# Optimization experiments

Hardware: AMD Instinct MI355X
Metric: run time of the kernel (lower is better)

Reference implementation:

```python
import jax, jax.numpy as jnp
import numpy as np

B, S, D, H = 2, 2048, 1024, 16
HD = D // H  # head_dim = 64
ROPE_BASE = 10000.0


def _rope_cos_sin(seq_len, head_dim, dtype=jnp.float32):
    inv_freq = 1.0 / (ROPE_BASE ** (jnp.arange(0, head_dim, 2, dtype=jnp.float32) / head_dim))
    t = jnp.arange(seq_len, dtype=jnp.float32)
    freqs = jnp.einsum('i,j->ij', t, inv_freq)          # [S, HD/2]
    emb = jnp.concatenate([freqs, freqs], axis=-1)       # [S, HD]
    return jnp.cos(emb).astype(dtype), jnp.sin(emb).astype(dtype)


def _rotate_half(x):
    x1, x2 = jnp.split(x, 2, axis=-1)
    return jnp.concatenate([-x2, x1], axis=-1)


def setup_inputs() -> dict:
    key = jax.random.key(0)
    ks = jax.random.split(key, 5)
    scale = 1.0 / np.sqrt(D)
    return {
        'hidden_states': jax.random.normal(ks[0], (B, S, D), dtype=jnp.float32),
        'Wq': jax.random.normal(ks[1], (D, D), dtype=jnp.float32) * scale,
        'Wk': jax.random.normal(ks[2], (D, D), dtype=jnp.float32) * scale,
        'Wv': jax.random.normal(ks[3], (D, D), dtype=jnp.float32) * scale,
        'Wo': jax.random.normal(ks[4], (D, D), dtype=jnp.float32) * scale,
    }


def reference(hidden_states, Wq, Wk, Wv, Wo):
    b, s, d = hidden_states.shape
    # torch nn.Linear(weight W) computes x @ W^T
    q = hidden_states @ Wq.T
    k = hidden_states @ Wk.T
    v = hidden_states @ Wv.T
    # [B, H, S, HD]
    q = q.reshape(b, s, H, HD).transpose(0, 2, 1, 3)
    k = k.reshape(b, s, H, HD).transpose(0, 2, 1, 3)
    v = v.reshape(b, s, H, HD).transpose(0, 2, 1, 3)
    cos, sin = _rope_cos_sin(s, HD, q.dtype)  # [S, HD]
    cos = cos[None, None]  # [1,1,S,HD]
    sin = sin[None, None]
    q = q * cos + _rotate_half(q) * sin
    k = k * cos + _rotate_half(k) * sin
    scale = HD ** -0.5
    attn = jnp.einsum('bhqd,bhkd->bhqk', q, k) * scale
    attn = jax.nn.softmax(attn.astype(jnp.float32), axis=-1).astype(q.dtype)
    out = jnp.einsum('bhqk,bhkd->bhqd', attn, v)
    out = out.transpose(0, 2, 1, 3).reshape(b, s, d)
    return out @ Wo.T
```

## Files before the change

### kernel.cpp

```cpp
#include <hip/hip_runtime.h>
#include <math.h>

constexpr int Bc = 2;
constexpr int Sc = 2048;
constexpr int Dc = 1024;
constexpr int Hc = 16;
constexpr int HDc = 64;

constexpr float QSC = 0.125f * 1.4426950408889634f;

typedef __attribute__((ext_vector_type(8))) short bf16x8;
typedef __attribute__((ext_vector_type(4))) float f32x4;
typedef __attribute__((ext_vector_type(4))) unsigned short us4;
typedef __attribute__((ext_vector_type(2))) unsigned int u32x2;
typedef __attribute__((ext_vector_type(4))) unsigned int u32x4;

typedef const __attribute__((address_space(1))) unsigned int* gp_t;
typedef __attribute__((address_space(3))) unsigned int* lp_t;

__device__ __forceinline__ unsigned f2bf(float x) {
    unsigned u = __float_as_uint(x);
    return (u + 0x7FFFu + ((u >> 16) & 1u)) >> 16;
}

__device__ __forceinline__ void split2(float x, unsigned short& h, unsigned short& l) {
    unsigned hh = f2bf(x);
    h = (unsigned short)hh;
    l = (unsigned short)f2bf(x - __uint_as_float(hh << 16));
}

#if __has_builtin(__builtin_amdgcn_permlane32_swap)
__device__ __forceinline__ void plswap32(unsigned& a, unsigned& b) {
    u32x2 r = __builtin_amdgcn_permlane32_swap(a, b, false, false);
    a = r.x; b = r.y;
}
#else
__device__ __forceinline__ void plswap32(unsigned& a, unsigned& b) {
    asm volatile("v_permlane32_swap_b32 %0, %1" : "+v"(a), "+v"(b));
}
#endif
#if __has_builtin(__builtin_amdgcn_permlane16_swap)
__device__ __forceinline__ void plswap16(unsigned& a, unsigned& b) {
    u32x2 r = __builtin_amdgcn_permlane16_swap(a, b, false, false);
    a = r.x; b = r.y;
}
#else
__device__ __forceinline__ void plswap16(unsigned& a, unsigned& b) {
    asm volatile("v_permlane16_swap_b32 %0, %1" : "+v"(a), "+v"(b));
}
#endif

__device__ __forceinline__ void exppack(const f32x4& sv, unsigned& w0, unsigned& w1) {
    unsigned u0 = __float_as_uint(__builtin_amdgcn_exp2f(sv[0]));
    unsigned u1 = __float_as_uint(__builtin_amdgcn_exp2f(sv[1]));
    unsigned u2 = __float_as_uint(__builtin_amdgcn_exp2f(sv[2]));
    unsigned u3 = __float_as_uint(__builtin_amdgcn_exp2f(sv[3]));
    w0 = __builtin_amdgcn_perm(u1, u0, 0x07060302u);
    w1 = __builtin_amdgcn_perm(u3, u2, 0x07060302u);
}

__global__ void rope_table(float* __restrict__ ct, float* __restrict__ st_) {
    int id = blockIdx.x * 256 + threadIdx.x;
    int s = id >> 5;
    int i = id & 31;
    double invf = pow(10000.0, -(double)i / 32.0);
    double ang = (double)s * invf;
    ct[id] = (float)cos(ang);
    st_[id] = (float)sin(ang);
}

__global__ void split_xw(const float* __restrict__ x,
                         const float* __restrict__ Wq, const float* __restrict__ Wk,
                         const float* __restrict__ Wv, const float* __restrict__ Wo,
                         unsigned short* __restrict__ xh,
                         unsigned short* __restrict__ whAll, unsigned short* __restrict__ wlAll) {
    int y = blockIdx.y;
    const float* src;
    unsigned short* h;
    unsigned short* l = nullptr;
    int n;
    if (y == 0) { src = x; h = xh; n = 1 << 22; }
    else {
        src = (y == 1) ? Wq : (y == 2) ? Wk : (y == 3) ? Wv : Wo;
        h = whAll + (size_t)(y - 1) * (1 << 20);
        if (y == 4) l = wlAll + (size_t)3 * (1 << 20);
        n = 1 << 20;
    }
    int i = (blockIdx.x * 256 + threadIdx.x) * 4;
    if (i >= n) return;
    float4 v = *(const float4*)(src + i);
    us4 hh;
    ((unsigned short*)&hh)[0] = (unsigned short)f2bf(v.x);
    ((unsigned short*)&hh)[1] = (unsigned short)f2bf(v.y);
    ((unsigned short*)&hh)[2] = (unsigned short)f2bf(v.z);
    ((unsigned short*)&hh)[3] = (unsigned short)f2bf(v.w);
    *(us4*)(h + i) = hh;
    if (l) {
        us4 ll;
        const float* vp = (const float*)&v;
#pragma unroll
        for (int e = 0; e < 4; e++) {
            unsigned short hi = ((unsigned short*)&hh)[e];
            ((unsigned short*)&ll)[e] =
                (unsigned short)f2bf(vp[e] - __uint_as_float((unsigned)hi << 16));
        }
        *(us4*)(l + i) = ll;
    }
}

__global__ __launch_bounds__(512, 4) void gemm_qkv9(
    const unsigned short* __restrict__ Ah,
    const unsigned short* __restrict__ whAll,
    unsigned short* __restrict__ Qh,
    unsigned short* __restrict__ Kh,
    unsigned short* __restrict__ Vh,
    const float* __restrict__ ct, const float* __restrict__ st_) {
    constexpr int K = 1024;
    __shared__ __align__(16) unsigned short As[2][8192], Bs[2][8192];

    const int t = threadIdx.x;
    const int lane = t & 63;
    const int wave = t >> 6;
    const int l15 = lane & 15;
    const int quad = lane >> 4;
    const int wr = wave >> 1;
    const int wc = wave & 1;
    const int m0 = blockIdx.x * 128;
    const int n0 = blockIdx.y * 128;
    const int z = blockIdx.z;
    const unsigned short* Wh = whAll + (size_t)z * (1 << 20);

    const int c0 = t,        r0 = c0 >> 3, s0 = c0 & 7;
    const int c1 = t + 512,  r1 = c1 >> 3, s1 = c1 & 7;
    const unsigned short* gA0 = Ah + (size_t)(m0 + r0) * K + (s0 ^ (r0 & 7)) * 8;
    const unsigned short* gA1 = Ah + (size_t)(m0 + r1) * K + (s1 ^ (r1 & 7)) * 8;
    const unsigned short* gB0 = Wh + (size_t)(n0 + r0) * K + (s0 ^ (r0 & 7)) * 8;
    const unsigned short* gB1 = Wh + (size_t)(n0 + r1) * K + (s1 ^ (r1 & 7)) * 8;
    const int d0 = c0 * 8, d1 = c1 * 8;

    f32x4 acc[2][4];
#pragma unroll
    for (int i = 0; i < 2; i++)
#pragma unroll
        for (int j = 0; j < 4; j++) acc[i][j] = (f32x4){0.f, 0.f, 0.f, 0.f};

#define STGQ(X) do {                                                                       \
        const int _ko = (X) * 64;                                                          \
        const int _bf = (X) & 1;                                                           \
        __builtin_amdgcn_global_load_lds((gp_t)(gA0 + _ko), (lp_t)(&As[_bf][d0]), 16, 0, 0); \
        __builtin_amdgcn_global_load_lds((gp_t)(gA1 + _ko), (lp_t)(&As[_bf][d1]), 16, 0, 0); \
        __builtin_amdgcn_global_load_lds((gp_t)(gB0 + _ko), (lp_t)(&Bs[_bf][d0]), 16, 0, 0); \
        __builtin_amdgcn_global_load_lds((gp_t)(gB1 + _ko), (lp_t)(&Bs[_bf][d1]), 16, 0, 0); \
    } while (0)

    STGQ(0);

    for (int it = 0; it < 16; ++it) {
        __syncthreads();
        if (it + 1 < 16) STGQ(it + 1);
        const unsigned short* a = &As[it & 1][0];
        const unsigned short* bb = &Bs[it & 1][0];
#pragma unroll
        for (int ks = 0; ks < 2; ks++) {
            bf16x8 ah[2], bh[4];
#pragma unroll
            for (int i = 0; i < 2; i++) {
                int row = wr * 32 + i * 16 + l15;
                ah[i] = *(const bf16x8*)&a[row * 64 + ((ks * 4 + quad) ^ (row & 7)) * 8];
            }
#pragma unroll
            for (int j = 0; j < 4; j++) {
                int row = wc * 64 + j * 16 + l15;
                bh[j] = *(const bf16x8*)&bb[row * 64 + ((ks * 4 + quad) ^ (row & 7)) * 8];
            }
#pragma unroll
            for (int i = 0; i < 2; i++)
#pragma unroll
                for (int j = 0; j < 4; j++)
                    acc[i][j] = __builtin_amdgcn_mfma_f32_16x16x32_bf16(ah[i], bh[j], acc[i][j], 0, 0, 0);
        }
    }
#undef STGQ

    const int hcol = blockIdx.y * 2 + wc;
    if (z == 2) {
#pragma unroll
        for (int i = 0; i < 2; i++) {
            int m_base = m0 + wr * 32 + i * 16 + quad * 4;
            int bbk = m_base >> 11;
            int T = (m_base & (Sc - 1)) >> 6;
            int ii = (2 * wr + i) & 3;
            int kk = ii >> 1;
            int qd = ((ii & 1) << 1) | (quad >> 1);
            int tj = (quad & 1) * 4;
            size_t tilebase = (((size_t)(bbk * Hc + hcol)) * 32 + T) * 4096;
#pragma unroll
            for (int jj = 0; jj < 4; jj++) {
                int d = jj * 16 + l15;
                size_t off = tilebase + (size_t)(((kk * 4 + qd) * 64 + d) * 8 + tj);
                us4 v4;
#pragma unroll
                for (int r = 0; r < 4; r++)
                    ((unsigned short*)&v4)[r] = (unsigned short)f2bf(acc[i][jj][r]);
                *(us4*)(Vh + off) = v4;
            }
        }
    } else {
#pragma unroll
        for (int i = 0; i < 2; i++)
#pragma unroll
            for (int r = 0; r < 4; r++) {
                int m = m0 + wr * 32 + i * 16 + quad * 4 + r;
                int bbk = m >> 11, s = m & (Sc - 1);
#pragma unroll
                for (int jp = 0; jp < 2; jp++) {
                    int d = jp * 16 + l15;
                    float cs = ct[s * 32 + d];
                    float sn = st_[s * 32 + d];
                    float x0 = acc[i][jp][r];
                    float x1 = acc[i][jp + 2][r];
                    float y0 = x0 * cs - x1 * sn;
                    float y1 = x1 * cs + x0 * sn;
                    if (z == 0) {
                        size_t rowb = (((size_t)(bbk * Hc + hcol)) * Sc + s) * HDc;
                        Qh[rowb + d]      = (unsigned short)f2bf(y0 * QSC);
                        Qh[rowb + d + 32] = (unsigned short)f2bf(y1 * QSC);
                    } else {
                        int T = s >> 6, tok = s & 63;
                        size_t tb = (((size_t)(bbk * Hc + hcol)) * 32 + T) * 8;
                        size_t off0 = ((tb + (d >> 3)) * 64 + tok) * 8 + (d & 7);
                        size_t off1 = ((tb + (d >> 3) + 4) * 64 + tok) * 8 + (d & 7);
                        Kh[off0] = (unsigned short)f2bf(y0);
                        Kh[off1] = (unsigned short)f2bf(y1);
                    }
                }
            }
    }
}

__global__ __launch_bounds__(512) void attn11(
    const unsigned short* __restrict__ Qh,
    const unsigned short* __restrict__ Kh,
    const unsigned short* __restrict__ Vh,
    unsigned short* __restrict__ AOh, unsigned short* __restrict__ AOl) {
    __shared__ __align__(16) unsigned short KsH[3 * 4096], VtH[3 * 4096];

    const int t = threadIdx.x;
    const int lane = t & 63;
    const int wave = t >> 6;
    const int l = lane & 15;
    const int quad = lane >> 4;
    const int id = blockIdx.x;
    const int bh = (id & 7) * 4 + (id >> 7);
    const int qt = (id >> 3) & 15;
    const int q0 = qt * 128;
    const int b = bh >> 4;
    const int hh = bh & 15;

    const bf16x8 ONES8 = {(short)0x3F80, (short)0x3F80, (short)0x3F80, (short)0x3F80,
                          (short)0x3F80, (short)0x3F80, (short)0x3F80, (short)0x3F80};

    bf16x8 qf[2];
    {
        size_t rowb = ((size_t)bh * Sc + q0 + wave * 16 + l) * HDc;
#pragma unroll
        for (int ks = 0; ks < 2; ks++)
            qf[ks] = *(const bf16x8*)(Qh + rowb + ks * 32 + quad * 8);
    }

    f32x4 o[4], lac;
    lac = (f32x4){0.f, 0.f, 0.f, 0.f};
#pragma unroll
    for (int i = 0; i < 4; i++) o[i] = (f32x4){0.f, 0.f, 0.f, 0.f};

    const int tensor = wave >> 2;
    const int coff0 = (wave * 2) & 7;
    unsigned short* larr = tensor ? VtH : KsH;
    const unsigned short* gT =
        (tensor ? Vh : Kh) + (size_t)bh * Sc * HDc + coff0 * 512 + lane * 8;

#pragma unroll
    for (int q = 0; q < 2; q++)
        __builtin_amdgcn_global_load_lds(
            (gp_t)(gT + q * 512),
            (lp_t)(larr + coff0 * 512 + q * 512),
            16, 0, 0);

    int bc = 0;
    for (int kt = 0; kt < 32; kt++) {
        if (kt + 1 < 32) {
            int nb = bc + 1; if (nb == 3) nb = 0;
            const unsigned short* g = gT + (size_t)(kt + 1) * 4096;
            unsigned short* dst = larr + nb * 4096 + coff0 * 512;
#pragma unroll
            for (int q = 0; q < 2; q++)
                __builtin_amdgcn_global_load_lds(
                    (gp_t)(g + q * 512),
                    (lp_t)(dst + q * 512),
                    16, 0, 0);
            asm volatile("s_waitcnt vmcnt(2)" ::: "memory");
        } else {
            asm volatile("s_waitcnt vmcnt(0)" ::: "memory");
        }
        __builtin_amdgcn_s_barrier();
        const unsigned short* Kbuf = KsH + bc * 4096;
        const unsigned short* Vbuf = VtH + bc * 4096;

        f32x4 s[4];
#pragma unroll
        for (int tt = 0; tt < 4; tt++) s[tt] = (f32x4){0.f, 0.f, 0.f, 0.f};
        __builtin_amdgcn_s_setprio(1);
#pragma unroll
        for (int ks = 0; ks < 2; ks++)
#pragma unroll
            for (int tt = 0; tt < 4; tt++) {
                bf16x8 kf = *(const bf16x8*)&Kbuf[((ks * 4 + quad) * 64 + tt * 16 + l) * 8];
                s[tt] = __builtin_amdgcn_mfma_f32_16x16x32_bf16(kf, qf[ks], s[tt], 0, 0, 0);
            }
        __builtin_amdgcn_s_setprio(0);

        bf16x8 pf[2];
#pragma unroll
        for (int ttp = 0; ttp < 2; ttp++) {
            unsigned A0, A1, B0, B1;
            exppack(s[2 * ttp], A0, A1);
            exppack(s[2 * ttp + 1], B0, B1);
            plswap32(A0, B0);
            plswap16(A0, B0);
            plswap32(A1, B1);
            plswap16(A1, B1);
            u32x4 fw = {A0, A1, B0, B1};
            bf16x8 p8 = __builtin_bit_cast(bf16x8, fw);
            pf[ttp] = p8;
            lac = __builtin_amdgcn_mfma_f32_16x16x32_bf16(ONES8, p8, lac, 0, 0, 0);
        }

        __builtin_amdgcn_s_setprio(1);
#pragma unroll
        for (int kk = 0; kk < 2; kk++)
#pragma unroll
            for (int dd = 0; dd < 4; dd++) {
                bf16x8 vf = *(const bf16x8*)
                    &Vbuf[(size_t)((kk * 4 + quad) * 64 + dd * 16 + l) * 8];
                o[dd] = __builtin_amdgcn_mfma_f32_16x16x32_bf16(vf, pf[kk], o[dd], 0, 0, 0);
            }
        __builtin_amdgcn_s_setprio(0);
        if (++bc == 3) bc = 0;
    }

    {
        float inv = 1.f / lac[0];
        int q = q0 + wave * 16 + l;
        size_t rowb = ((size_t)b * Sc + q) * Dc + hh * HDc + quad * 4;
#pragma unroll
        for (int dd = 0; dd < 4; dd++) {
            us4 h4, l4;
#pragma unroll
            for (int r = 0; r < 4; r++)
                split2(o[dd][r] * inv,
                       ((unsigned short*)&h4)[r], ((unsigned short*)&l4)[r]);
            *(us4*)(AOh + rowb + dd * 16) = h4;
            *(us4*)(AOl + rowb + dd * 16) = l4;
        }
    }
}

__global__ __launch_bounds__(512, 4) void gemm_out9(
    const unsigned short* __restrict__ Ah, const unsigned short* __restrict__ Al,
    const unsigned short* __restrict__ Wh, const unsigned short* __restrict__ Wl,
    float* __restrict__ C0, float* __restrict__ C1) {
    constexpr int K = 1024;
    __shared__ __align__(16) unsigned short AsH[2][4096], AsL[2][4096],
                                            BsH[2][4096], BsL[2][4096];

    const int t = threadIdx.x;
    const int lane = t & 63;
    const int wave = t >> 6;
    const int l15 = lane & 15;
    const int quad = lane >> 4;
    const int wr = wave >> 1;
    const int wc = wave & 1;
    const int m0 = blockIdx.x * 128;
    const int n0 = blockIdx.y * 128;
    const int k0 = blockIdx.z * 512;
    float* __restrict__ C = blockIdx.z ? C1 : C0;

    const int rr = t >> 2, ss = t & 3;
    const int gc = (ss ^ (rr & 3)) * 8;
    const unsigned short* gah = Ah + (size_t)(m0 + rr) * K + k0 + gc;
    const unsigned short* gal = Al + (size_t)(m0 + rr) * K + k0 + gc;
    const unsigned short* gbh = Wh + (size_t)(n0 + rr) * K + k0 + gc;
    const unsigned short* gbl = Wl + (size_t)(n0 + rr) * K + k0 + gc;
    const int dd_ = t * 8;

    f32x4 acc[2][4];
#pragma unroll
    for (int i = 0; i < 2; i++)
#pragma unroll
        for (int j = 0; j < 4; j++) acc[i][j] = (f32x4){0.f, 0.f, 0.f, 0.f};

#define STGO(X) do {                                                                       \
        const int _ko = (X) * 32;                                                          \
        const int _bf = (X) & 1;                                                           \
        __builtin_amdgcn_global_load_lds((gp_t)(gah + _ko), (lp_t)(&AsH[_bf][dd_]), 16, 0, 0); \
        __builtin_amdgcn_global_load_lds((gp_t)(gal + _ko), (lp_t)(&AsL[_bf][dd_]), 16, 0, 0); \
        __builtin_amdgcn_global_load_lds((gp_t)(gbh + _ko), (lp_t)(&BsH[_bf][dd_]), 16, 0, 0); \
        __builtin_amdgcn_global_load_lds((gp_t)(gbl + _ko), (lp_t)(&BsL[_bf][dd_]), 16, 0, 0); \
    } while (0)

    STGO(0);

    for (int it = 0; it < 16; ++it) {
        __syncthreads();
        if (it + 1 < 16) STGO(it + 1);
        const int bf = it & 1;
        bf16x8 ah[2], al[2], bh[4], bl[4];
#pragma unroll
        for (int i = 0; i < 2; i++) {
            int row = wr * 32 + i * 16 + l15;
            int ra = row * 32 + (quad ^ (row & 3)) * 8;
            ah[i] = *(const bf16x8*)&AsH[bf][ra];
            al[i] = *(const bf16x8*)&AsL[bf][ra];
        }
#pragma unroll
        for (int j = 0; j < 4; j++) {
            int row = wc * 64 + j * 16 + l15;
            int rb = row * 32 + (quad ^ (row & 3)) * 8;
            bh[j] = *(const bf16x8*)&BsH[bf][rb];
            bl[j] = *(const bf16x8*)&BsL[bf][rb];
        }
#pragma unroll
        for (int i = 0; i < 2; i++)
#pragma unroll
            for (int j = 0; j < 4; j++) {
                acc[i][j] = __builtin_amdgcn_mfma_f32_16x16x32_bf16(ah[i], bh[j], acc[i][j], 0, 0, 0);
                acc[i][j] = __builtin_amdgcn_mfma_f32_16x16x32_bf16(al[i], bh[j], acc[i][j], 0, 0, 0);
                acc[i][j] = __builtin_amdgcn_mfma_f32_16x16x32_bf16(ah[i], bl[j], acc[i][j], 0, 0, 0);
            }
    }
#undef STGO

#pragma unroll
    for (int i = 0; i < 2; i++)
#pragma unroll
        for (int j = 0; j < 4; j++)
#pragma unroll
            for (int r = 0; r < 4; r++) {
                int m = m0 + wr * 32 + i * 16 + quad * 4 + r;
                int n = n0 + wc * 64 + j * 16 + l15;
                C[(size_t)m * Dc + n] = acc[i][j][r];
            }
}

__global__ void add_partial(float* __restrict__ out, const float* __restrict__ p1) {
    int i = (blockIdx.x * 256 + threadIdx.x) * 4;
    float4 a = *(const float4*)(out + i);
    float4 b = *(const float4*)(p1 + i);
    a.x += b.x; a.y += b.y; a.z += b.z; a.w += b.w;
    *(float4*)(out + i) = a;
}

extern "C" void kernel_launch(void* const* d_in, const int* in_sizes, int n_in,
                              void* d_out, int out_size, void* d_ws, size_t ws_size,
                              hipStream_t stream) {
    const float* x  = (const float*)d_in[0];
    const float* Wq = (const float*)d_in[1];
    const float* Wk = (const float*)d_in[2];
    const float* Wv = (const float*)d_in[3];
    const float* Wo = (const float*)d_in[4];
    float* out = (float*)d_out;

    unsigned short* usw = (unsigned short*)d_ws;
    const size_t M4 = (size_t)1 << 22;
    unsigned short* whAll = usw;
    unsigned short* wlAll = usw + M4;
    unsigned short* xh = usw + 2 * M4;
    unsigned short* xl = usw + 3 * M4;
    unsigned short* Qh = usw + 4 * M4;
    unsigned short* Kh = usw + 5 * M4;
    unsigned short* Vh = usw + 6 * M4;
    float* ct = (float*)(usw + 7 * M4);
    float* st_ = ct + (size_t)Sc * 32;
    unsigned short* AOh = xh;
    unsigned short* AOl = xl;
    float* P1 = (float*)Qh;

    rope_table<<<dim3((Sc * 32) / 256), dim3(256), 0, stream>>>(ct, st_);
    split_xw<<<dim3(4096, 5), dim3(256), 0, stream>>>(x, Wq, Wk, Wv, Wo, xh, whAll, wlAll);
    gemm_qkv9<<<dim3(32, 8, 3), dim3(512), 0, stream>>>(
        xh, whAll, Qh, Kh, Vh, ct, st_);
    attn11<<<dim3(512), dim3(512), 0, stream>>>(Qh, Kh, Vh, AOh, AOl);
    gemm_out9<<<dim3(32, 8, 2), dim3(512), 0, stream>>>(
        AOh, AOl, whAll + 3 * (1 << 20), wlAll + 3 * (1 << 20), out, P1);
    add_partial<<<dim3(4096), dim3(256), 0, stream>>>(out, P1);
}
```

Before: 197.5 us.

## Enlarge QKV GEMM tile to 256x256 with split-K-half LDS pipeline

Replaces the 128x128 QKV projection GEMM tile with a 256x256 tile per block, where each wave computes a 128x64 sub-tile, raising arithmetic intensity per LDS load. The K loop is restructured into half-slabs of 32 with explicit vmcnt waits, raw s_barriers and setprio around the MFMA bursts, so that global-to-LDS prefetch overlaps compute. The grid shrinks from 768 blocks to 192, which fills fewer workgroups than the GPU has CUs, and the larger accumulator set raises register pressure (launch bounds drop to 2 blocks per CU). The hand-tuned waitcnt schedule is fragile and depends on the exact number of outstanding loads.

```diff
diff --git a/kernel.cpp b/kernel.cpp
--- a/kernel.cpp
+++ b/kernel.cpp
@@ -108,7 +108,7 @@
     }
 }
 
-__global__ __launch_bounds__(512, 4) void gemm_qkv9(
+__global__ __launch_bounds__(512, 2) void gemm_qkv8(
     const unsigned short* __restrict__ Ah,
     const unsigned short* __restrict__ whAll,
     unsigned short* __restrict__ Qh,
@@ -116,80 +116,116 @@
     unsigned short* __restrict__ Vh,
     const float* __restrict__ ct, const float* __restrict__ st_) {
     constexpr int K = 1024;
-    __shared__ __align__(16) unsigned short As[2][8192], Bs[2][8192];
+    __shared__ __align__(16) unsigned short As[2][16384], Bs[2][16384];
 
     const int t = threadIdx.x;
     const int lane = t & 63;
     const int wave = t >> 6;
     const int l15 = lane & 15;
     const int quad = lane >> 4;
-    const int wr = wave >> 1;
-    const int wc = wave & 1;
-    const int m0 = blockIdx.x * 128;
-    const int n0 = blockIdx.y * 128;
+    const int wr = wave >> 2;
+    const int wc = wave & 3;
+    const int m0 = blockIdx.x * 256;
+    const int n0 = blockIdx.y * 256;
     const int z = blockIdx.z;
     const unsigned short* Wh = whAll + (size_t)z * (1 << 20);
 
-    const int c0 = t,        r0 = c0 >> 3, s0 = c0 & 7;
-    const int c1 = t + 512,  r1 = c1 >> 3, s1 = c1 & 7;
-    const unsigned short* gA0 = Ah + (size_t)(m0 + r0) * K + (s0 ^ (r0 & 7)) * 8;
-    const unsigned short* gA1 = Ah + (size_t)(m0 + r1) * K + (s1 ^ (r1 & 7)) * 8;
-    const unsigned short* gB0 = Wh + (size_t)(n0 + r0) * K + (s0 ^ (r0 & 7)) * 8;
-    const unsigned short* gB1 = Wh + (size_t)(n0 + r1) * K + (s1 ^ (r1 & 7)) * 8;
-    const int d0 = c0 * 8, d1 = c1 * 8;
-
-    f32x4 acc[2][4];
-#pragma unroll
-    for (int i = 0; i < 2; i++)
+    const int row0 = t >> 2;
+    const int gch = (t & 3) ^ (row0 & 3);
+    const unsigned short* gA0 = Ah + (size_t)(m0 + row0) * K + gch * 8;
+    const unsigned short* gA1 = Ah + (size_t)(m0 + row0 + 128) * K + gch * 8;
+    const unsigned short* gB0 = Wh + (size_t)(n0 + row0) * K + gch * 8;
+    const unsigned short* gB1 = Wh + (size_t)(n0 + row0 + 128) * K + gch * 8;
+    const int d0 = t * 8;
+    const int d1 = (t + 512) * 8;
+
+    f32x4 acc[8][4];
+#pragma unroll
+    for (int i = 0; i < 8; i++)
 #pragma unroll
         for (int j = 0; j < 4; j++) acc[i][j] = (f32x4){0.f, 0.f, 0.f, 0.f};
-
-#define STGQ(X) do {                                                                       \
-        const int _ko = (X) * 64;                                                          \
-        const int _bf = (X) & 1;                                                           \
-        __builtin_amdgcn_global_load_lds((gp_t)(gA0 + _ko), (lp_t)(&As[_bf][d0]), 16, 0, 0); \
-        __builtin_amdgcn_global_load_lds((gp_t)(gA1 + _ko), (lp_t)(&As[_bf][d1]), 16, 0, 0); \
-        __builtin_amdgcn_global_load_lds((gp_t)(gB0 + _ko), (lp_t)(&Bs[_bf][d0]), 16, 0, 0); \
-        __builtin_amdgcn_global_load_lds((gp_t)(gB1 + _ko), (lp_t)(&Bs[_bf][d1]), 16, 0, 0); \
+    bf16x8 af[8];
+
+#define STG(g0, g1, LARR, X, KH) do {                                                      \
+        const int _ko = (X) * 64 + (KH) * 32;                                              \
+        const int _lo = (KH) * 8192;                                                       \
+        __builtin_amdgcn_global_load_lds((gp_t)((g0) + _ko),                               \
+            (lp_t)(&LARR[(X) & 1][d0 + _lo]), 16, 0, 0);                                   \
+        __builtin_amdgcn_global_load_lds((gp_t)((g1) + _ko),                               \
+            (lp_t)(&LARR[(X) & 1][d1 + _lo]), 16, 0, 0);                                   \
     } while (0)
 
-    STGQ(0);
-
-    for (int it = 0; it < 16; ++it) {
-        __syncthreads();
-        if (it + 1 < 16) STGQ(it + 1);
-        const unsigned short* a = &As[it & 1][0];
-        const unsigned short* bb = &Bs[it & 1][0];
-#pragma unroll
-        for (int ks = 0; ks < 2; ks++) {
-            bf16x8 ah[2], bh[4];
-#pragma unroll
-            for (int i = 0; i < 2; i++) {
-                int row = wr * 32 + i * 16 + l15;
-                ah[i] = *(const bf16x8*)&a[row * 64 + ((ks * 4 + quad) ^ (row & 7)) * 8];
-            }
-#pragma unroll
-            for (int j = 0; j < 4; j++) {
-                int row = wc * 64 + j * 16 + l15;
-                bh[j] = *(const bf16x8*)&bb[row * 64 + ((ks * 4 + quad) ^ (row & 7)) * 8];
-            }
-#pragma unroll
-            for (int i = 0; i < 2; i++)
-#pragma unroll
-                for (int j = 0; j < 4; j++)
-                    acc[i][j] = __builtin_amdgcn_mfma_f32_16x16x32_bf16(ah[i], bh[j], acc[i][j], 0, 0, 0);
-        }
-    }
-#undef STGQ
-
-    const int hcol = blockIdx.y * 2 + wc;
+#define VM10 asm volatile("s_waitcnt vmcnt(10)" ::: "memory")
+#define VM8  asm volatile("s_waitcnt vmcnt(8)" ::: "memory")
+#define VM4  asm volatile("s_waitcnt vmcnt(4)" ::: "memory")
+#define VM0  asm volatile("s_waitcnt vmcnt(0)" ::: "memory")
+
+#define CPH(BUF, KS, J0, RA, PRE) do {                                                     \
+        PRE;                                                                               \
+        asm volatile("s_barrier" ::: "memory");                                            \
+        const unsigned short* _a = &As[(BUF)][(KS) * 8192];                                \
+        const unsigned short* _b = &Bs[(BUF)][(KS) * 8192];                                \
+        if (RA) {                                                                          \
+            _Pragma("unroll")                                                              \
+            for (int _i = 0; _i < 8; _i++) {                                               \
+                int _row = wr * 128 + _i * 16 + l15;                                       \
+                af[_i] = *(const bf16x8*)&_a[_row * 32 + (quad ^ (_row & 3)) * 8];         \
+            }                                                                              \
+        }                                                                                  \
+        int _rb0 = wc * 64 + (J0) * 16 + l15;                                              \
+        int _rb1 = wc * 64 + ((J0) + 1) * 16 + l15;                                        \
+        bf16x8 _bf0 = *(const bf16x8*)&_b[_rb0 * 32 + (quad ^ (_rb0 & 3)) * 8];            \
+        bf16x8 _bf1 = *(const bf16x8*)&_b[_rb1 * 32 + (quad ^ (_rb1 & 3)) * 8];            \
+        __builtin_amdgcn_s_setprio(1);                                                     \
+        _Pragma("unroll")                                                                  \
+        for (int _i = 0; _i < 8; _i++) {                                                   \
+            acc[_i][(J0)]     = __builtin_amdgcn_mfma_f32_16x16x32_bf16(af[_i], _bf0,      \
+                                    acc[_i][(J0)], 0, 0, 0);                               \
+            acc[_i][(J0) + 1] = __builtin_amdgcn_mfma_f32_16x16x32_bf16(af[_i], _bf1,      \
+                                    acc[_i][(J0) + 1], 0, 0, 0);                           \
+        }                                                                                  \
+        __builtin_amdgcn_s_setprio(0);                                                     \
+        asm volatile("s_barrier" ::: "memory");                                            \
+    } while (0)
+
+    STG(gA0, gA1, As, 0, 0); STG(gB0, gB1, Bs, 0, 0);
+    STG(gA0, gA1, As, 0, 1); STG(gB0, gB1, Bs, 0, 1);
+    STG(gA0, gA1, As, 1, 0); STG(gB0, gB1, Bs, 1, 0);
+
+    for (int e = 0; e < 14; e += 2) {
+        CPH(0, 0, 0, 1, STG(gA0, gA1, As, e + 1, 1); VM10);
+        CPH(0, 0, 2, 0, STG(gB0, gB1, Bs, e + 1, 1));
+        CPH(0, 1, 0, 1, STG(gA0, gA1, As, e + 2, 0); VM10);
+        CPH(0, 1, 2, 0, STG(gB0, gB1, Bs, e + 2, 0));
+        CPH(1, 0, 0, 1, STG(gA0, gA1, As, e + 2, 1); VM10);
+        CPH(1, 0, 2, 0, STG(gB0, gB1, Bs, e + 2, 1));
+        CPH(1, 1, 0, 1, STG(gA0, gA1, As, e + 3, 0); VM10);
+        CPH(1, 1, 2, 0, STG(gB0, gB1, Bs, e + 3, 0));
+    }
+    CPH(0, 0, 0, 1, STG(gA0, gA1, As, 15, 1); VM10);
+    CPH(0, 0, 2, 0, STG(gB0, gB1, Bs, 15, 1));
+    CPH(0, 1, 0, 1, VM8);
+    CPH(0, 1, 2, 0, );
+    CPH(1, 0, 0, 1, VM4);
+    CPH(1, 0, 2, 0, );
+    CPH(1, 1, 0, 1, VM0);
+    CPH(1, 1, 2, 0, );
+
+#undef CPH
+#undef STG
+#undef VM10
+#undef VM8
+#undef VM4
+#undef VM0
+
+    const int hcol = blockIdx.y * 4 + wc;
     if (z == 2) {
 #pragma unroll
-        for (int i = 0; i < 2; i++) {
-            int m_base = m0 + wr * 32 + i * 16 + quad * 4;
+        for (int i = 0; i < 8; i++) {
+            int m_base = m0 + wr * 128 + i * 16 + quad * 4;
             int bbk = m_base >> 11;
             int T = (m_base & (Sc - 1)) >> 6;
-            int ii = (2 * wr + i) & 3;
+            int ii = i & 3;
             int kk = ii >> 1;
             int qd = ((ii & 1) << 1) | (quad >> 1);
             int tj = (quad & 1) * 4;
@@ -207,10 +243,10 @@
         }
     } else {
 #pragma unroll
-        for (int i = 0; i < 2; i++)
+        for (int i = 0; i < 8; i++)
 #pragma unroll
             for (int r = 0; r < 4; r++) {
-                int m = m0 + wr * 32 + i * 16 + quad * 4 + r;
+                int m = m0 + wr * 128 + i * 16 + quad * 4 + r;
                 int bbk = m >> 11, s = m & (Sc - 1);
 #pragma unroll
                 for (int jp = 0; jp < 2; jp++) {
@@ -487,7 +523,7 @@
 
     rope_table<<<dim3((Sc * 32) / 256), dim3(256), 0, stream>>>(ct, st_);
     split_xw<<<dim3(4096, 5), dim3(256), 0, stream>>>(x, Wq, Wk, Wv, Wo, xh, whAll, wlAll);
-    gemm_qkv9<<<dim3(32, 8, 3), dim3(512), 0, stream>>>(
+    gemm_qkv8<<<dim3(16, 4, 3), dim3(512), 0, stream>>>(
         xh, whAll, Qh, Kh, Vh, ct, st_);
     attn11<<<dim3(512), dim3(512), 0, stream>>>(Qh, Kh, Vh, AOh, AOl);
     gemm_out9<<<dim3(32, 8, 2), dim3(512), 0, stream>>>(
```

New measurement: 215.4 us. +9.0%, slower.
